# Kernel tuning notes

Measured on AMD Instinct MI355X. Metric: run time of the kernel, lower is better.

The kernel has to match this reference:

```python
import jax, jax.numpy as jnp
import numpy as np

B, T, H, L, NB, NL = 32, 512, 256, 2048, 256, 4
F0_MIN, F0_MAX = 0.0, 1.0
E_MIN, E_MAX = 0.0, 1.0


def setup_inputs() -> dict:
    key = jax.random.key(0)
    ks = jax.random.split(key, 12)
    s = 1.0 / np.sqrt(H)
    return {
        "x": jax.random.normal(ks[0], (B, T, H), jnp.float32),
        "src_seq": jax.random.uniform(ks[1], (B, T, 3), jnp.float32, 1.0, 8.0),
        "duration_target": jax.random.randint(ks[2], (B, T), 0, 7, jnp.int32),
        "pitch_target": jax.random.uniform(ks[3], (B, L), jnp.float32),
        "energy_target": jax.random.uniform(ks[4], (B, L), jnp.float32),
        "src_mask": jnp.zeros((B, T), bool),
        "max_len": L,
        "dur_W": jax.random.normal(ks[5], (NL, H, H), jnp.float32) * s,
        "dur_b": jnp.zeros((NL, H), jnp.float32),
        "dur_w": jax.random.normal(ks[6], (H,), jnp.float32) * s,
        "dur_b2": jnp.zeros((1,), jnp.float32),
        "pit_W": jax.random.normal(ks[7], (NL, H, H), jnp.float32) * s,
        "pit_b": jnp.zeros((NL, H), jnp.float32),
        "pit_w": jax.random.normal(ks[8], (H,), jnp.float32) * s,
        "pit_b2": jnp.zeros((1,), jnp.float32),
        "en_W": jax.random.normal(ks[9], (NL, H, H), jnp.float32) * s,
        "en_b": jnp.zeros((NL, H), jnp.float32),
        "en_w": jax.random.normal(ks[10], (H,), jnp.float32) * s,
        "en_b2": jnp.zeros((1,), jnp.float32),
        "pitch_emb": jax.random.normal(ks[11], (2 * NB, H), jnp.float32),
        "energy_emb": jax.random.normal(jax.random.fold_in(key, 99), (2 * NB, H), jnp.float32),
    }


def _predictor(h, W, b, w, b2, mask):
    # stand-in for Decoder(n_layers=4) + Linear(H, 1) head
    for i in range(NL):
        h = jax.nn.relu(jnp.einsum('blh,hk->blk', h, W[i]) + b[i])
    out = jnp.einsum('blh,h->bl', h, w) + b2[0]
    return jnp.where(mask, 0.0, out)


def _length_regulate(x, dur, max_len):
    # cumsum-based repeat_interleave: frame m maps to token searchsorted(cumsum(dur), m, 'right')
    cum = jnp.cumsum(dur, axis=1)                      # [B, T]
    mel_len = jnp.minimum(cum[:, -1], max_len)         # [B]
    frames = jnp.arange(max_len)                       # [L]
    idx = jax.vmap(lambda c: jnp.searchsorted(c, frames, side='right'))(cum)
    idx = jnp.clip(idx, 0, x.shape[1] - 1)             # [B, L]
    out = jnp.take_along_axis(x, idx[:, :, None], axis=1)  # [B, L, H]
    mel_mask = frames[None, :] >= mel_len[:, None]     # True = padding
    out = out * (~mel_mask)[:, :, None]
    return out, mel_len, mel_mask


def reference(x, src_seq, duration_target, pitch_target, energy_target, src_mask, max_len,
              dur_W, dur_b, dur_w, dur_b2, pit_W, pit_b, pit_w, pit_b2,
              en_W, en_b, en_w, en_b2, pitch_emb, energy_emb):
    # duration predictor: LengthPredictor = decoder + linear + tanh, scaled by note lengths
    d = _predictor(x, dur_W, dur_b, dur_w, dur_b2, src_mask)
    log_duration_prediction = (jnp.tanh(d) + 1.0) * src_seq[:, :, 2]

    # length regulator (training path: duration_target provided)
    xe, mel_len, mel_mask = _length_regulate(x, duration_target, max_len)

    pitch_prediction = jax.nn.relu(_predictor(xe, pit_W, pit_b, pit_w, pit_b2, mel_mask))
    p_idx = jnp.ceil((pitch_target - F0_MIN) / (F0_MAX - F0_MIN) * NB).astype(jnp.int32)
    p_emb = pitch_emb[p_idx]                            # [B, L, H]

    energy_prediction = _predictor(xe, en_W, en_b, en_w, en_b2, mel_mask)
    e_idx = jnp.ceil((energy_target - E_MIN) / (E_MAX - E_MIN) * NB).astype(jnp.int32)
    e_emb = energy_emb[e_idx]                           # [B, L, H]

    out = xe + p_emb + e_emb
    return out, log_duration_prediction, pitch_prediction, energy_prediction, mel_len, mel_mask
```

## Files before the change

kernel.cpp:

```cpp
#include <hip/hip_runtime.h>

typedef _Float16 half_t;
typedef _Float16 half4 __attribute__((ext_vector_type(4)));
typedef _Float16 half8 __attribute__((ext_vector_type(8)));
typedef float floatx4 __attribute__((ext_vector_type(4)));

#define HST 264
#define B_ 32
#define T_ 512
#define H_ 256
#define L_ 2048

__global__ __launch_bounds__(256) void setup_kernel(
    const int* __restrict__ dur,
    const float* __restrict__ pitch_t,
    const float* __restrict__ energy_t,
    const float* __restrict__ dur_W,
    const float* __restrict__ pit_W,
    const float* __restrict__ en_W,
    half_t* __restrict__ Wp,
    int* __restrict__ idx_ws,
    int* __restrict__ pi_ws,
    int* __restrict__ ei_ws,
    int* __restrict__ ml_ws,
    float* __restrict__ out4,
    float* __restrict__ out5) {
  __shared__ int cum_l[T_];
  __shared__ int ml_s;
  int bid = blockIdx.x;
  int tid = threadIdx.x;

  if (bid >= 128) {
    int g = (bid - 128) * 256 + tid;
    int lane = g & 63;
    int t = g >> 6;
    int nt = t & 15;
    int kk = (t >> 4) & 7;
    int layer = (t >> 7) & 3;
    int pred = t >> 9;
    const float* W = (pred == 0 ? dur_W : (pred == 1 ? pit_W : en_W)) + layer * 65536;
    int n = nt * 16 + (lane & 15);
    int k0 = kk * 32 + (lane >> 4) * 8;
    half8 o;
#pragma unroll
    for (int j = 0; j < 8; ++j) o[j] = (half_t)W[(k0 + j) * 256 + n];
    int c = (pred * 4 + layer) * 16 + nt;
    *(half8*)&Wp[(size_t)c * 4096 + kk * 512 + lane * 8] = o;
    return;
  }

  int b = bid >> 2;
  int chunk = bid & 3;
  if (tid < 64) {
    int l = tid;
    const int* dr = dur + b * T_;
    int v[8];
    int base = l * 8;
#pragma unroll
    for (int j = 0; j < 8; ++j) v[j] = dr[base + j];
#pragma unroll
    for (int j = 1; j < 8; ++j) v[j] += v[j - 1];
    int tot = v[7];
    int inc = tot;
    for (int d = 1; d < 64; d <<= 1) {
      int t = __shfl_up(inc, d);
      if (l >= d) inc += t;
    }
    int excl = inc - tot;
#pragma unroll
    for (int j = 0; j < 8; ++j) cum_l[base + j] = excl + v[j];
    if (l == 63) {
      int mel = min(inc, L_);
      ml_s = mel;
      if (chunk == 0) {
        ml_ws[b] = mel;
        out4[b] = (float)mel;
      }
    }
  }
  __syncthreads();
  int ml = ml_s;
#pragma unroll
  for (int j = 0; j < 2; ++j) {
    int m = chunk * 512 + j * 256 + tid;
    int lo = 0;
#pragma unroll
    for (int sh = 8; sh >= 0; --sh) {
      int c = lo + (1 << sh);
      if (c <= T_ && cum_l[c - 1] <= m) lo = c;
    }
    int idx = min(lo, T_ - 1);
    int g = b * L_ + m;
    idx_ws[g] = idx;
    pi_ws[g] = (int)ceilf(pitch_t[g] * 256.0f);
    ei_ws[g] = (int)ceilf(energy_t[g] * 256.0f);
    out5[g] = (m >= ml) ? 1.0f : 0.0f;
  }
}

__device__ __forceinline__ void stage16(const void* g, void* l) {
  __builtin_amdgcn_global_load_lds(
      (const __attribute__((address_space(1))) void*)g,
      (__attribute__((address_space(3))) void*)l, 16, 0, 0);
}

__global__ __launch_bounds__(128, 2) void predictor_kernel(
    const float* __restrict__ x,
    const half_t* __restrict__ Wp,
    const float* __restrict__ dur_b, const float* __restrict__ dur_w, const float* __restrict__ dur_b2,
    const float* __restrict__ pit_b, const float* __restrict__ pit_w, const float* __restrict__ pit_b2,
    const float* __restrict__ en_b,  const float* __restrict__ en_w,  const float* __restrict__ en_b2,
    const int* __restrict__ idx_ws, const int* __restrict__ pi_ws, const int* __restrict__ ei_ws,
    const int* __restrict__ mlw,
    const float* __restrict__ src_seq, const unsigned char* __restrict__ src_mask,
    const float* __restrict__ pemb, const float* __restrict__ eemb,
    float* __restrict__ out0, float* __restrict__ out1,
    float* __restrict__ out2, float* __restrict__ out3) {
  __shared__ half_t hlds[64 * HST];
  __shared__ half_t wldsw[8192];

  int bid = blockIdx.x;
  int mode, blk;
  const half_t* W; const float* bias; const float* wh; const float* b2p; float* outp;
  if (bid < 1024)      { mode = 1; blk = bid;        W = Wp + 262144; bias = pit_b; wh = pit_w; b2p = pit_b2; outp = out2; }
  else if (bid < 2048) { mode = 2; blk = bid - 1024; W = Wp + 524288; bias = en_b;  wh = en_w;  b2p = en_b2;  outp = out3; }
  else                 { mode = 0; blk = bid - 2048; W = Wp;          bias = dur_b; wh = dur_w; b2p = dur_b2; outp = out1; }

  int tid = threadIdx.x;
  int wv = tid >> 6, lane = tid & 63;
  int mi = lane & 15, qi = lane >> 4;
  int wrow0 = wv * 32;
  int brow0 = blk * 64;

  const char* Wb = (const char*)W;
  char* wbb = (char*)&wldsw[0];

#define STAGE(c)                                                        \
  {                                                                     \
    const char* gsrc = Wb + (size_t)(c) * 8192 + wv * 1024 + lane * 16; \
    char* ldst = wbb + ((c) & 1) * 8192 + wv * 1024;                    \
    stage16(gsrc,        ldst);                                         \
    stage16(gsrc + 2048, ldst + 2048);                                  \
    stage16(gsrc + 4096, ldst + 4096);                                  \
    stage16(gsrc + 6144, ldst + 6144);                                  \
  }

  STAGE(0);

  if (mode == 0) {
    for (int it = 0; it < 32; ++it) {
      int rl = wrow0 + it;
      const float4 xv = *(const float4*)&x[(size_t)(brow0 + rl) * H_ + lane * 4];
      half4 h4;
      h4[0] = (half_t)xv.x; h4[1] = (half_t)xv.y;
      h4[2] = (half_t)xv.z; h4[3] = (half_t)xv.w;
      *(half4*)&hlds[rl * HST + lane * 4] = h4;
    }
  } else {
    int b = brow0 >> 11;
    int m0 = brow0 & (L_ - 1);
    int ml = mlw[b];
    for (int it = 0; it < 32; ++it) {
      int rl = wrow0 + it;
      int m = m0 + rl;
      int g = b * L_ + m;
      float4 xv = {0.f, 0.f, 0.f, 0.f};
      if (m < ml) {
        int ir = idx_ws[g];
        xv = *(const float4*)&x[((size_t)(b * T_ + ir)) * H_ + lane * 4];
      }
      if (mode == 1) {
        const float4 pv = *(const float4*)&pemb[(size_t)pi_ws[g] * H_ + lane * 4];
        const float4 ev = *(const float4*)&eemb[(size_t)ei_ws[g] * H_ + lane * 4];
        floatx4 o;
        o[0] = xv.x + pv.x + ev.x;
        o[1] = xv.y + pv.y + ev.y;
        o[2] = xv.z + pv.z + ev.z;
        o[3] = xv.w + pv.w + ev.w;
        __builtin_nontemporal_store(o, (floatx4*)&out0[(size_t)g * H_ + lane * 4]);
      }
      half4 h4;
      h4[0] = (half_t)xv.x; h4[1] = (half_t)xv.y;
      h4[2] = (half_t)xv.z; h4[3] = (half_t)xv.w;
      *(half4*)&hlds[rl * HST + lane * 4] = h4;
    }
  }
  __syncthreads();

#pragma unroll 1
  for (int layer = 0; layer < 4; ++layer) {
    const float* bl = bias + layer * 256;

    half8 hf[2][8];
#pragma unroll
    for (int mt = 0; mt < 2; ++mt)
#pragma unroll
      for (int kk = 0; kk < 8; ++kk)
        hf[mt][kk] = *(const half8*)&hlds[(wrow0 + mt * 16 + mi) * HST + kk * 32 + qi * 8];

#pragma unroll 2
    for (int nt = 0; nt < 16; ++nt) {
      int c = layer * 16 + nt;
      if (c < 63) STAGE(c + 1);

      const half_t* wb = &wldsw[(c & 1) * 4096];
      half8 w[8];
#pragma unroll
      for (int kk = 0; kk < 8; ++kk)
        w[kk] = *(const half8*)&wb[kk * 512 + lane * 8];

      floatx4 acc0 = {0.f, 0.f, 0.f, 0.f};
      floatx4 acc1 = {0.f, 0.f, 0.f, 0.f};
#pragma unroll
      for (int kk = 0; kk < 8; ++kk) {
        acc0 = __builtin_amdgcn_mfma_f32_16x16x32_f16(w[kk], hf[0][kk], acc0, 0, 0, 0);
        acc1 = __builtin_amdgcn_mfma_f32_16x16x32_f16(w[kk], hf[1][kk], acc1, 0, 0, 0);
      }
      const float4 bv = *(const float4*)&bl[nt * 16 + qi * 4];
      int colbase = nt * 16 + qi * 4;
      half4 h40, h41;
      h40[0] = (half_t)fmaxf(acc0[0] + bv.x, 0.f);
      h40[1] = (half_t)fmaxf(acc0[1] + bv.y, 0.f);
      h40[2] = (half_t)fmaxf(acc0[2] + bv.z, 0.f);
      h40[3] = (half_t)fmaxf(acc0[3] + bv.w, 0.f);
      h41[0] = (half_t)fmaxf(acc1[0] + bv.x, 0.f);
      h41[1] = (half_t)fmaxf(acc1[1] + bv.y, 0.f);
      h41[2] = (half_t)fmaxf(acc1[2] + bv.z, 0.f);
      h41[3] = (half_t)fmaxf(acc1[3] + bv.w, 0.f);
      *(half4*)&hlds[(wrow0 + mi) * HST + colbase] = h40;
      *(half4*)&hlds[(wrow0 + 16 + mi) * HST + colbase] = h41;

      __syncthreads();
    }
  }

  {
    int r = lane >> 1, hf2 = lane & 1;
    int rl = wrow0 + r;
    float sum = 0.f;
    const half_t* hrow = &hlds[rl * HST + hf2 * 128];
    const float* whp = wh + hf2 * 128;
#pragma unroll
    for (int j = 0; j < 16; ++j) {
      half8 hv = *(const half8*)&hrow[j * 8];
#pragma unroll
      for (int u = 0; u < 8; ++u) sum += (float)hv[u] * whp[j * 8 + u];
    }
    sum += __shfl_xor(sum, 1);
    if (hf2 == 0) {
      int row = brow0 + rl;
      float d = sum + b2p[0];
      if (mode == 0) {
        if (src_mask[row]) d = 0.f;
        float s2 = src_seq[(size_t)row * 3 + 2];
        outp[row] = (tanhf(d) + 1.0f) * s2;
      } else {
        int b = row >> 11;
        int m = row & (L_ - 1);
        float v = (m >= mlw[b]) ? 0.f : d;
        outp[row] = (mode == 1) ? fmaxf(v, 0.f) : v;
      }
    }
  }
#undef STAGE
}

extern "C" void kernel_launch(void* const* d_in, const int* in_sizes, int n_in,
                              void* d_out, int out_size, void* d_ws, size_t ws_size,
                              hipStream_t stream) {
  const float* x        = (const float*)d_in[0];
  const float* src_seq  = (const float*)d_in[1];
  const int*   durt     = (const int*)d_in[2];
  const float* pitcht   = (const float*)d_in[3];
  const float* energyt  = (const float*)d_in[4];
  const unsigned char* src_mask = (const unsigned char*)d_in[5];
  const float* dur_W  = (const float*)d_in[7];
  const float* dur_b  = (const float*)d_in[8];
  const float* dur_w  = (const float*)d_in[9];
  const float* dur_b2 = (const float*)d_in[10];
  const float* pit_W  = (const float*)d_in[11];
  const float* pit_b  = (const float*)d_in[12];
  const float* pit_w  = (const float*)d_in[13];
  const float* pit_b2 = (const float*)d_in[14];
  const float* en_W   = (const float*)d_in[15];
  const float* en_b   = (const float*)d_in[16];
  const float* en_w   = (const float*)d_in[17];
  const float* en_b2  = (const float*)d_in[18];
  const float* pemb   = (const float*)d_in[19];
  const float* eemb   = (const float*)d_in[20];

  float* out0 = (float*)d_out;
  float* out1 = out0 + 16777216;
  float* out2 = out1 + 16384;
  float* out3 = out2 + 65536;
  float* out4 = out3 + 65536;
  float* out5 = out4 + 32;

  int* idx_ws = (int*)d_ws;
  int* pi_ws  = idx_ws + 65536;
  int* ei_ws  = pi_ws + 65536;
  int* ml_ws  = ei_ws + 65536;
  half_t* Wp  = (half_t*)((char*)d_ws + 786560);

  setup_kernel<<<dim3(512), dim3(256), 0, stream>>>(
      durt, pitcht, energyt, dur_W, pit_W, en_W, Wp,
      idx_ws, pi_ws, ei_ws, ml_ws, out4, out5);
  predictor_kernel<<<dim3(2304), dim3(128), 0, stream>>>(
      x, Wp,
      dur_b, dur_w, dur_b2,
      pit_b, pit_w, pit_b2,
      en_b, en_w, en_b2,
      idx_ws, pi_ws, ei_ws, ml_ws, src_seq, src_mask, pemb, eemb,
      out0, out1, out2, out3);
}
```

Measured before the change: 278.0 us.

## Triple-buffer weight staging, re-layout activations in LDS, fuse head dot into last layer

```diff
diff --git a/kernel.cpp b/kernel.cpp
--- a/kernel.cpp
+++ b/kernel.cpp
@@ -5,7 +5,6 @@
 typedef _Float16 half8 __attribute__((ext_vector_type(8)));
 typedef float floatx4 __attribute__((ext_vector_type(4)));
 
-#define HST 264
 #define B_ 32
 #define T_ 512
 #define H_ 256
@@ -104,7 +103,7 @@
       (__attribute__((address_space(3))) void*)l, 16, 0, 0);
 }
 
-__global__ __launch_bounds__(128, 2) void predictor_kernel(
+__global__ __launch_bounds__(128, 1) void predictor_kernel(
     const float* __restrict__ x,
     const half_t* __restrict__ Wp,
     const float* __restrict__ dur_b, const float* __restrict__ dur_w, const float* __restrict__ dur_b2,
@@ -116,8 +115,8 @@
     const float* __restrict__ pemb, const float* __restrict__ eemb,
     float* __restrict__ out0, float* __restrict__ out1,
     float* __restrict__ out2, float* __restrict__ out3) {
-  __shared__ half_t hlds[64 * HST];
-  __shared__ half_t wldsw[8192];
+  __shared__ half_t hlds[16384];
+  __shared__ half_t wlds[12288];
 
   int bid = blockIdx.x;
   int mode, blk;
@@ -133,19 +132,19 @@
   int brow0 = blk * 64;
 
   const char* Wb = (const char*)W;
-  char* wbb = (char*)&wldsw[0];
-
-#define STAGE(c)                                                        \
-  {                                                                     \
-    const char* gsrc = Wb + (size_t)(c) * 8192 + wv * 1024 + lane * 16; \
-    char* ldst = wbb + ((c) & 1) * 8192 + wv * 1024;                    \
-    stage16(gsrc,        ldst);                                         \
-    stage16(gsrc + 2048, ldst + 2048);                                  \
-    stage16(gsrc + 4096, ldst + 4096);                                  \
-    stage16(gsrc + 6144, ldst + 6144);                                  \
-  }
-
-  STAGE(0);
+
+#define STAGE(c, s)                                                          \
+  {                                                                          \
+    const char* gsrc = Wb + (size_t)(c) * 8192 + wv * 4096 + lane * 16;      \
+    char* ldst = (char*)wlds + (s) * 8192 + wv * 4096;                       \
+    stage16(gsrc,        ldst);                                              \
+    stage16(gsrc + 1024, ldst + 1024);                                       \
+    stage16(gsrc + 2048, ldst + 2048);                                       \
+    stage16(gsrc + 3072, ldst + 3072);                                       \
+  }
+
+  STAGE(0, 0);
+  STAGE(1, 1);
 
   if (mode == 0) {
     for (int it = 0; it < 32; ++it) {
@@ -154,7 +153,7 @@
       half4 h4;
       h4[0] = (half_t)xv.x; h4[1] = (half_t)xv.y;
       h4[2] = (half_t)xv.z; h4[3] = (half_t)xv.w;
-      *(half4*)&hlds[rl * HST + lane * 4] = h4;
+      *(half4*)&hlds[(lane >> 3) * 2048 + rl * 32 + (lane & 7) * 4] = h4;
     }
   } else {
     int b = brow0 >> 11;
@@ -182,84 +181,100 @@
       half4 h4;
       h4[0] = (half_t)xv.x; h4[1] = (half_t)xv.y;
       h4[2] = (half_t)xv.z; h4[3] = (half_t)xv.w;
-      *(half4*)&hlds[rl * HST + lane * 4] = h4;
+      *(half4*)&hlds[(lane >> 3) * 2048 + rl * 32 + (lane & 7) * 4] = h4;
     }
   }
   __syncthreads();
 
+  half8 hf[2][8];
+  float p0 = 0.f, p1 = 0.f;
+  int sl = 0;
+
 #pragma unroll 1
-  for (int layer = 0; layer < 4; ++layer) {
+  for (int c = 0; c < 64; ++c) {
+    int layer = c >> 4, nt = c & 15;
+
+    if (nt == 0) {
+#pragma unroll
+      for (int mt = 0; mt < 2; ++mt)
+#pragma unroll
+        for (int kk = 0; kk < 8; ++kk)
+          hf[mt][kk] = *(const half8*)&hlds[kk * 2048 + (wrow0 + mt * 16 + mi) * 32 + qi * 8];
+    }
+
+    const half_t* wb = &wlds[sl * 4096];
+    half8 w[8];
+#pragma unroll
+    for (int kk = 0; kk < 8; ++kk)
+      w[kk] = *(const half8*)&wb[kk * 512 + lane * 8];
+
+    asm volatile("s_waitcnt lgkmcnt(0)" ::: "memory");
+    __builtin_amdgcn_sched_barrier(0);
+    int sl2 = sl + 2; if (sl2 >= 3) sl2 -= 3;
+    if (c < 62) {
+      STAGE(c + 2, sl2);
+      asm volatile("s_waitcnt vmcnt(4)" ::: "memory");
+    } else {
+      asm volatile("s_waitcnt vmcnt(0)" ::: "memory");
+    }
+    __builtin_amdgcn_sched_barrier(0);
+    __builtin_amdgcn_s_barrier();
+    __builtin_amdgcn_sched_barrier(0);
+
+    floatx4 a0l = {0.f, 0.f, 0.f, 0.f}, a0h = a0l, a1l = a0l, a1h = a0l;
+#pragma unroll
+    for (int kk = 0; kk < 4; ++kk) {
+      a0l = __builtin_amdgcn_mfma_f32_16x16x32_f16(w[kk], hf[0][kk], a0l, 0, 0, 0);
+      a1l = __builtin_amdgcn_mfma_f32_16x16x32_f16(w[kk], hf[1][kk], a1l, 0, 0, 0);
+    }
+#pragma unroll
+    for (int kk = 4; kk < 8; ++kk) {
+      a0h = __builtin_amdgcn_mfma_f32_16x16x32_f16(w[kk], hf[0][kk], a0h, 0, 0, 0);
+      a1h = __builtin_amdgcn_mfma_f32_16x16x32_f16(w[kk], hf[1][kk], a1h, 0, 0, 0);
+    }
+
     const float* bl = bias + layer * 256;
-
-    half8 hf[2][8];
-#pragma unroll
-    for (int mt = 0; mt < 2; ++mt)
-#pragma unroll
-      for (int kk = 0; kk < 8; ++kk)
-        hf[mt][kk] = *(const half8*)&hlds[(wrow0 + mt * 16 + mi) * HST + kk * 32 + qi * 8];
-
-#pragma unroll 2
-    for (int nt = 0; nt < 16; ++nt) {
-      int c = layer * 16 + nt;
-      if (c < 63) STAGE(c + 1);
-
-      const half_t* wb = &wldsw[(c & 1) * 4096];
-      half8 w[8];
-#pragma unroll
-      for (int kk = 0; kk < 8; ++kk)
-        w[kk] = *(const half8*)&wb[kk * 512 + lane * 8];
-
-      floatx4 acc0 = {0.f, 0.f, 0.f, 0.f};
-      floatx4 acc1 = {0.f, 0.f, 0.f, 0.f};
-#pragma unroll
-      for (int kk = 0; kk < 8; ++kk) {
-        acc0 = __builtin_amdgcn_mfma_f32_16x16x32_f16(w[kk], hf[0][kk], acc0, 0, 0, 0);
-        acc1 = __builtin_amdgcn_mfma_f32_16x16x32_f16(w[kk], hf[1][kk], acc1, 0, 0, 0);
-      }
-      const float4 bv = *(const float4*)&bl[nt * 16 + qi * 4];
-      int colbase = nt * 16 + qi * 4;
+    const float4 bv = *(const float4*)&bl[nt * 16 + qi * 4];
+    float v00 = fmaxf(a0l[0] + a0h[0] + bv.x, 0.f);
+    float v01 = fmaxf(a0l[1] + a0h[1] + bv.y, 0.f);
+    float v02 = fmaxf(a0l[2] + a0h[2] + bv.z, 0.f);
+    float v03 = fmaxf(a0l[3] + a0h[3] + bv.w, 0.f);
+    float v10 = fmaxf(a1l[0] + a1h[0] + bv.x, 0.f);
+    float v11 = fmaxf(a1l[1] + a1h[1] + bv.y, 0.f);
+    float v12 = fmaxf(a1l[2] + a1h[2] + bv.z, 0.f);
+    float v13 = fmaxf(a1l[3] + a1h[3] + bv.w, 0.f);
+
+    if (layer < 3) {
       half4 h40, h41;
-      h40[0] = (half_t)fmaxf(acc0[0] + bv.x, 0.f);
-      h40[1] = (half_t)fmaxf(acc0[1] + bv.y, 0.f);
-      h40[2] = (half_t)fmaxf(acc0[2] + bv.z, 0.f);
-      h40[3] = (half_t)fmaxf(acc0[3] + bv.w, 0.f);
-      h41[0] = (half_t)fmaxf(acc1[0] + bv.x, 0.f);
-      h41[1] = (half_t)fmaxf(acc1[1] + bv.y, 0.f);
-      h41[2] = (half_t)fmaxf(acc1[2] + bv.z, 0.f);
-      h41[3] = (half_t)fmaxf(acc1[3] + bv.w, 0.f);
-      *(half4*)&hlds[(wrow0 + mi) * HST + colbase] = h40;
-      *(half4*)&hlds[(wrow0 + 16 + mi) * HST + colbase] = h41;
-
-      __syncthreads();
-    }
-  }
-
-  {
-    int r = lane >> 1, hf2 = lane & 1;
-    int rl = wrow0 + r;
-    float sum = 0.f;
-    const half_t* hrow = &hlds[rl * HST + hf2 * 128];
-    const float* whp = wh + hf2 * 128;
-#pragma unroll
-    for (int j = 0; j < 16; ++j) {
-      half8 hv = *(const half8*)&hrow[j * 8];
-#pragma unroll
-      for (int u = 0; u < 8; ++u) sum += (float)hv[u] * whp[j * 8 + u];
-    }
-    sum += __shfl_xor(sum, 1);
-    if (hf2 == 0) {
-      int row = brow0 + rl;
-      float d = sum + b2p[0];
-      if (mode == 0) {
-        if (src_mask[row]) d = 0.f;
-        float s2 = src_seq[(size_t)row * 3 + 2];
-        outp[row] = (tanhf(d) + 1.0f) * s2;
-      } else {
-        int b = row >> 11;
-        int m = row & (L_ - 1);
-        float v = (m >= mlw[b]) ? 0.f : d;
-        outp[row] = (mode == 1) ? fmaxf(v, 0.f) : v;
-      }
+      h40[0] = (half_t)v00; h40[1] = (half_t)v01; h40[2] = (half_t)v02; h40[3] = (half_t)v03;
+      h41[0] = (half_t)v10; h41[1] = (half_t)v11; h41[2] = (half_t)v12; h41[3] = (half_t)v13;
+      int base = (nt >> 1) * 2048 + (nt & 1) * 16 + qi * 4;
+      *(half4*)&hlds[base + (wrow0 + mi) * 32] = h40;
+      *(half4*)&hlds[base + (wrow0 + 16 + mi) * 32] = h41;
+    } else {
+      const float4 wv4 = *(const float4*)&wh[nt * 16 + qi * 4];
+      p0 += v00 * wv4.x + v01 * wv4.y + v02 * wv4.z + v03 * wv4.w;
+      p1 += v10 * wv4.x + v11 * wv4.y + v12 * wv4.z + v13 * wv4.w;
+    }
+
+    sl = (sl == 2) ? 0 : sl + 1;
+  }
+
+  p0 += __shfl_xor(p0, 16); p0 += __shfl_xor(p0, 32);
+  p1 += __shfl_xor(p1, 16); p1 += __shfl_xor(p1, 32);
+  if (qi < 2) {
+    float sum = (qi == 0) ? p0 : p1;
+    int row = brow0 + wrow0 + ((qi == 0) ? mi : 16 + mi);
+    float d = sum + b2p[0];
+    if (mode == 0) {
+      if (src_mask[row]) d = 0.f;
+      float s2 = src_seq[(size_t)row * 3 + 2];
+      outp[row] = (tanhf(d) + 1.0f) * s2;
+    } else {
+      int b = row >> 11;
+      int m = row & (L_ - 1);
+      float v = (m >= mlw[b]) ? 0.f : d;
+      outp[row] = (mode == 1) ? fmaxf(v, 0.f) : v;
     }
   }
 #undef STAGE
```

After: 348.4 us. +25.3%, slower.

## Split predictor block across four waves with larger weight chunks and fused head

Applied to the files above, without the earlier changes.

```diff
diff --git a/kernel.cpp b/kernel.cpp
--- a/kernel.cpp
+++ b/kernel.cpp
@@ -104,7 +104,7 @@
       (__attribute__((address_space(3))) void*)l, 16, 0, 0);
 }
 
-__global__ __launch_bounds__(128, 2) void predictor_kernel(
+__global__ __launch_bounds__(256) void predictor_kernel(
     const float* __restrict__ x,
     const half_t* __restrict__ Wp,
     const float* __restrict__ dur_b, const float* __restrict__ dur_w, const float* __restrict__ dur_b2,
@@ -117,7 +117,7 @@
     float* __restrict__ out0, float* __restrict__ out1,
     float* __restrict__ out2, float* __restrict__ out3) {
   __shared__ half_t hlds[64 * HST];
-  __shared__ half_t wldsw[8192];
+  __shared__ half_t wlds[16384];
 
   int bid = blockIdx.x;
   int mode, blk;
@@ -129,26 +129,25 @@
   int tid = threadIdx.x;
   int wv = tid >> 6, lane = tid & 63;
   int mi = lane & 15, qi = lane >> 4;
-  int wrow0 = wv * 32;
+  int wrow0 = wv * 16;
   int brow0 = blk * 64;
 
   const char* Wb = (const char*)W;
-  char* wbb = (char*)&wldsw[0];
-
-#define STAGE(c)                                                        \
-  {                                                                     \
-    const char* gsrc = Wb + (size_t)(c) * 8192 + wv * 1024 + lane * 16; \
-    char* ldst = wbb + ((c) & 1) * 8192 + wv * 1024;                    \
-    stage16(gsrc,        ldst);                                         \
-    stage16(gsrc + 2048, ldst + 2048);                                  \
-    stage16(gsrc + 4096, ldst + 4096);                                  \
-    stage16(gsrc + 6144, ldst + 6144);                                  \
-  }
-
-  STAGE(0);
+
+#define STAGE(cc, bf)                                                        \
+  {                                                                          \
+    const char* gsrc = Wb + (size_t)(cc) * 16384 + wv * 4096 + lane * 16;    \
+    char* ldst = (char*)wlds + (bf) * 32768 + wv * 4096;                     \
+    stage16(gsrc,        ldst);                                              \
+    stage16(gsrc + 1024, ldst + 1024);                                       \
+    stage16(gsrc + 2048, ldst + 2048);                                       \
+    stage16(gsrc + 3072, ldst + 3072);                                       \
+  }
+
+  STAGE(0, 0);
 
   if (mode == 0) {
-    for (int it = 0; it < 32; ++it) {
+    for (int it = 0; it < 16; ++it) {
       int rl = wrow0 + it;
       const float4 xv = *(const float4*)&x[(size_t)(brow0 + rl) * H_ + lane * 4];
       half4 h4;
@@ -160,7 +159,7 @@
     int b = brow0 >> 11;
     int m0 = brow0 & (L_ - 1);
     int ml = mlw[b];
-    for (int it = 0; it < 32; ++it) {
+    for (int it = 0; it < 16; ++it) {
       int rl = wrow0 + it;
       int m = m0 + rl;
       int g = b * L_ + m;
@@ -187,79 +186,89 @@
   }
   __syncthreads();
 
+  half8 hf[8];
+  float p = 0.f;
+
 #pragma unroll 1
-  for (int layer = 0; layer < 4; ++layer) {
+  for (int cc = 0; cc < 32; ++cc) {
+    int layer = cc >> 3, np = cc & 7;
     const float* bl = bias + layer * 256;
 
-    half8 hf[2][8];
-#pragma unroll
-    for (int mt = 0; mt < 2; ++mt)
-#pragma unroll
-      for (int kk = 0; kk < 8; ++kk)
-        hf[mt][kk] = *(const half8*)&hlds[(wrow0 + mt * 16 + mi) * HST + kk * 32 + qi * 8];
-
-#pragma unroll 2
-    for (int nt = 0; nt < 16; ++nt) {
-      int c = layer * 16 + nt;
-      if (c < 63) STAGE(c + 1);
-
-      const half_t* wb = &wldsw[(c & 1) * 4096];
+    float4 bvA = *(const float4*)&bl[(np * 2) * 16 + qi * 4];
+    float4 bvB = *(const float4*)&bl[(np * 2 + 1) * 16 + qi * 4];
+    float4 hwA = {0.f, 0.f, 0.f, 0.f}, hwB = {0.f, 0.f, 0.f, 0.f};
+    if (layer == 3) {
+      hwA = *(const float4*)&wh[(np * 2) * 16 + qi * 4];
+      hwB = *(const float4*)&wh[(np * 2 + 1) * 16 + qi * 4];
+    }
+
+    if (cc < 31) STAGE(cc + 1, (cc + 1) & 1);
+
+    if (np == 0) {
+#pragma unroll
+      for (int kk = 0; kk < 8; ++kk)
+        hf[kk] = *(const half8*)&hlds[(wrow0 + mi) * HST + kk * 32 + qi * 8];
+    }
+
+    const half_t* wb = &wlds[(cc & 1) * 16384];
+    {
       half8 w[8];
 #pragma unroll
       for (int kk = 0; kk < 8; ++kk)
         w[kk] = *(const half8*)&wb[kk * 512 + lane * 8];
-
-      floatx4 acc0 = {0.f, 0.f, 0.f, 0.f};
-      floatx4 acc1 = {0.f, 0.f, 0.f, 0.f};
-#pragma unroll
-      for (int kk = 0; kk < 8; ++kk) {
-        acc0 = __builtin_amdgcn_mfma_f32_16x16x32_f16(w[kk], hf[0][kk], acc0, 0, 0, 0);
-        acc1 = __builtin_amdgcn_mfma_f32_16x16x32_f16(w[kk], hf[1][kk], acc1, 0, 0, 0);
-      }
-      const float4 bv = *(const float4*)&bl[nt * 16 + qi * 4];
-      int colbase = nt * 16 + qi * 4;
-      half4 h40, h41;
-      h40[0] = (half_t)fmaxf(acc0[0] + bv.x, 0.f);
-      h40[1] = (half_t)fmaxf(acc0[1] + bv.y, 0.f);
-      h40[2] = (half_t)fmaxf(acc0[2] + bv.z, 0.f);
-      h40[3] = (half_t)fmaxf(acc0[3] + bv.w, 0.f);
-      h41[0] = (half_t)fmaxf(acc1[0] + bv.x, 0.f);
-      h41[1] = (half_t)fmaxf(acc1[1] + bv.y, 0.f);
-      h41[2] = (half_t)fmaxf(acc1[2] + bv.z, 0.f);
-      h41[3] = (half_t)fmaxf(acc1[3] + bv.w, 0.f);
-      *(half4*)&hlds[(wrow0 + mi) * HST + colbase] = h40;
-      *(half4*)&hlds[(wrow0 + 16 + mi) * HST + colbase] = h41;
-
-      __syncthreads();
-    }
-  }
-
-  {
-    int r = lane >> 1, hf2 = lane & 1;
-    int rl = wrow0 + r;
-    float sum = 0.f;
-    const half_t* hrow = &hlds[rl * HST + hf2 * 128];
-    const float* whp = wh + hf2 * 128;
-#pragma unroll
-    for (int j = 0; j < 16; ++j) {
-      half8 hv = *(const half8*)&hrow[j * 8];
-#pragma unroll
-      for (int u = 0; u < 8; ++u) sum += (float)hv[u] * whp[j * 8 + u];
-    }
-    sum += __shfl_xor(sum, 1);
-    if (hf2 == 0) {
-      int row = brow0 + rl;
-      float d = sum + b2p[0];
-      if (mode == 0) {
-        if (src_mask[row]) d = 0.f;
-        float s2 = src_seq[(size_t)row * 3 + 2];
-        outp[row] = (tanhf(d) + 1.0f) * s2;
+      floatx4 acc = {bvA.x, bvA.y, bvA.z, bvA.w};
+#pragma unroll
+      for (int kk = 0; kk < 8; ++kk)
+        acc = __builtin_amdgcn_mfma_f32_16x16x32_f16(w[kk], hf[kk], acc, 0, 0, 0);
+      int nt = np * 2;
+      if (layer < 3) {
+        half4 h4;
+        h4[0] = (half_t)fmaxf(acc[0], 0.f); h4[1] = (half_t)fmaxf(acc[1], 0.f);
+        h4[2] = (half_t)fmaxf(acc[2], 0.f); h4[3] = (half_t)fmaxf(acc[3], 0.f);
+        *(half4*)&hlds[(wrow0 + mi) * HST + nt * 16 + qi * 4] = h4;
       } else {
-        int b = row >> 11;
-        int m = row & (L_ - 1);
-        float v = (m >= mlw[b]) ? 0.f : d;
-        outp[row] = (mode == 1) ? fmaxf(v, 0.f) : v;
-      }
+        p += fmaxf(acc[0], 0.f) * hwA.x + fmaxf(acc[1], 0.f) * hwA.y
+           + fmaxf(acc[2], 0.f) * hwA.z + fmaxf(acc[3], 0.f) * hwA.w;
+      }
+    }
+    {
+      half8 w[8];
+#pragma unroll
+      for (int kk = 0; kk < 8; ++kk)
+        w[kk] = *(const half8*)&wb[4096 + kk * 512 + lane * 8];
+      floatx4 acc = {bvB.x, bvB.y, bvB.z, bvB.w};
+#pragma unroll
+      for (int kk = 0; kk < 8; ++kk)
+        acc = __builtin_amdgcn_mfma_f32_16x16x32_f16(w[kk], hf[kk], acc, 0, 0, 0);
+      int nt = np * 2 + 1;
+      if (layer < 3) {
+        half4 h4;
+        h4[0] = (half_t)fmaxf(acc[0], 0.f); h4[1] = (half_t)fmaxf(acc[1], 0.f);
+        h4[2] = (half_t)fmaxf(acc[2], 0.f); h4[3] = (half_t)fmaxf(acc[3], 0.f);
+        *(half4*)&hlds[(wrow0 + mi) * HST + nt * 16 + qi * 4] = h4;
+      } else {
+        p += fmaxf(acc[0], 0.f) * hwB.x + fmaxf(acc[1], 0.f) * hwB.y
+           + fmaxf(acc[2], 0.f) * hwB.z + fmaxf(acc[3], 0.f) * hwB.w;
+      }
+    }
+
+    __syncthreads();
+  }
+
+  p += __shfl_xor(p, 16);
+  p += __shfl_xor(p, 32);
+  if (qi == 0) {
+    int row = brow0 + wrow0 + mi;
+    float d = p + b2p[0];
+    if (mode == 0) {
+      if (src_mask[row]) d = 0.f;
+      float s2 = src_seq[(size_t)row * 3 + 2];
+      outp[row] = (tanhf(d) + 1.0f) * s2;
+    } else {
+      int b = row >> 11;
+      int m = row & (L_ - 1);
+      float v = (m >= mlw[b]) ? 0.f : d;
+      outp[row] = (mode == 1) ? fmaxf(v, 0.f) : v;
     }
   }
 #undef STAGE
@@ -305,7 +314,7 @@
   setup_kernel<<<dim3(512), dim3(256), 0, stream>>>(
       durt, pitcht, energyt, dur_W, pit_W, en_W, Wp,
       idx_ws, pi_ws, ei_ws, ml_ws, out4, out5);
-  predictor_kernel<<<dim3(2304), dim3(128), 0, stream>>>(
+  predictor_kernel<<<dim3(2304), dim3(256), 0, stream>>>(
       x, Wp,
       dur_b, dur_w, dur_b2,
       pit_b, pit_w, pit_b2,
```

Result: no change. 282.2 us (+1.5%).
